# Performance work log

Measured on AMD Instinct MI355X. Metric: run time of the kernel, lower is better.

## Reference

```python
import jax, jax.numpy as jnp
import numpy as np

EMBED_DIM = 256
IDX = 3
SLOT_NORM = True
NEG = -9e15


def setup_inputs() -> dict:
    key = jax.random.key(0)
    ks = jax.random.split(key, 7)
    B, S, D, N = 16, 8192, EMBED_DIM, 64
    return {
        "input_embedding": jax.random.normal(ks[0], (B, S, D), dtype=jnp.float32),
        "mask": jax.random.randint(ks[1], (B, N, S), 0, 2, dtype=jnp.int32),
        "Wv": jax.random.normal(ks[2], (D, D), dtype=jnp.float32) * 0.02,
        "bv": jax.random.normal(ks[3], (D,), dtype=jnp.float32) * 0.02,
        "Wk": jax.random.normal(ks[4], (D, D), dtype=jnp.float32) * 0.02,
        "bk": jax.random.normal(ks[5], (D,), dtype=jnp.float32) * 0.02,
        "queries": jax.random.normal(ks[6], (N, D), dtype=jnp.float32) * 0.02,
    }


def reference(input_embedding, mask, Wv, bv, Wk, bk, queries):
    # values/keys: [B, S, D] (torch Linear: x @ W.T + b)
    values = jnp.einsum("bsd,ed->bse", input_embedding, Wv) + bv
    keys = jnp.einsum("bsd,ed->bse", input_embedding, Wk) + bk
    # attn_logits: [B, N, S]
    logits = jnp.einsum("nd,bsd->bns", queries, keys) / jnp.sqrt(
        jnp.asarray(EMBED_DIM, dtype=keys.dtype)
    )
    logits = jnp.where(mask == 0, jnp.asarray(NEG, dtype=logits.dtype), logits)
    if SLOT_NORM:
        attn = jax.nn.softmax(logits, axis=-2)  # normalize over slots
        attn = attn / jnp.sum(attn, axis=-1, keepdims=True)
    else:
        attn = jax.nn.softmax(logits, axis=-1)
    attention = attn[:, IDX, :][:, None, :]  # [B, 1, S]
    out = jnp.matmul(attention, values)  # [B, 1, D]
    return out, attention
```

## Files before the change

kernel.cpp:

```cpp
#include <hip/hip_runtime.h>


#define B_ 16
#define S_ 8192
#define D_ 256
#define N_ 64
#define NEG_ (-9e15f)
#define LSTR 264

typedef __attribute__((ext_vector_type(8))) short s8_t;
typedef __attribute__((ext_vector_type(4))) float f4_t;
typedef unsigned int u32;
typedef unsigned short u16;

__device__ __forceinline__ u16 f2bf(float f) {
  u32 u = __builtin_bit_cast(u32, f);
  u += 0x7fffu + ((u >> 16) & 1u);
  return (u16)(u >> 16);
}
__device__ __forceinline__ float bflo(u32 p) { return __builtin_bit_cast(float, p << 16); }
__device__ __forceinline__ float bfhi(u32 p) { return __builtin_bit_cast(float, p & 0xffff0000u); }

__global__ void prep_qk(const float* __restrict__ queries, const float* __restrict__ Wk,
                        const float* __restrict__ bk, u16* __restrict__ qp,
                        float* __restrict__ qb) {
  const int n = blockIdx.x, d = threadIdx.x;
  const float* q = &queries[n * D_];
  float acc = 0.f;
  for (int e = 0; e < D_; ++e) acc = fmaf(q[e], Wk[e * D_ + d], acc);
  qp[n * D_ + d] = f2bf(acc);
  if (d == 0) {
    float s = 0.f;
    for (int e = 0; e < D_; ++e) s = fmaf(q[e], bk[e], s);
    qb[n] = s;
  }
}

__global__ __launch_bounds__(256, 2) void attn_main(
    const float* __restrict__ x, const int* __restrict__ mask,
    const u16* __restrict__ qp, const float* __restrict__ qb,
    float* __restrict__ wsum, float* __restrict__ denom, float* __restrict__ att) {
  __shared__ u16 q_lds[N_ * LSTR];
  __shared__ u16 in_lds[64 * LSTR];
  __shared__ u32 pm[4 * 64];

  const int t = threadIdx.x;
  const int lane = t & 63;
  const int w = t >> 6;
  const int c15 = lane & 15;
  const int g = lane >> 4;
  const int b = blockIdx.y;
  const int sbase = blockIdx.x * 256;

  {
    const int n = t >> 2, q = t & 3;
#pragma unroll
    for (int j = 0; j < 8; ++j)
      *(uint4*)&q_lds[n * LSTR + q * 64 + j * 8] = *(const uint4*)&qp[n * D_ + q * 64 + j * 8];
  }
  float qbv[4];
#pragma unroll
  for (int t4 = 0; t4 < 4; ++t4) qbv[t4] = qb[t4 * 16 + c15];

  f4_t wacc = {0.f, 0.f, 0.f, 0.f};
  float dacc = 0.f;

  for (int tt = 0; tt < 4; ++tt) {
    const int s0 = sbase + tt * 64;
    __syncthreads();
    {
      const int col = (t & 63) * 4;
#pragma unroll
      for (int it = 0; it < 16; ++it) {
        const int row = it * 4 + w;
        const float4 v = *(const float4*)&x[(((long)b * S_) + s0 + row) * D_ + col];
        uint2 h;
        h.x = (u32)f2bf(v.x) | ((u32)f2bf(v.y) << 16);
        h.y = (u32)f2bf(v.z) | ((u32)f2bf(v.w) << 16);
        *(uint2*)&in_lds[row * LSTR + col] = h;
      }
      const int s = t & 63, p = t >> 6;
      const int* mrow = mask + ((long)b * N_ + p * 16) * S_ + s0 + s;
      u32 bits = 0;
#pragma unroll
      for (int i = 0; i < 16; ++i) bits |= (u32)(mrow[i * S_] != 0) << i;
      pm[p * 64 + s] = bits;
    }
    __syncthreads();

    f4_t acc[4] = {{0.f,0.f,0.f,0.f},{0.f,0.f,0.f,0.f},{0.f,0.f,0.f,0.f},{0.f,0.f,0.f,0.f}};
    const u16* arow = &in_lds[(16 * w + c15) * LSTR + g * 8];
    const u16* br0 = &q_lds[(0 + c15) * LSTR + g * 8];
    const u16* br1 = &q_lds[(16 + c15) * LSTR + g * 8];
    const u16* br2 = &q_lds[(32 + c15) * LSTR + g * 8];
    const u16* br3 = &q_lds[(48 + c15) * LSTR + g * 8];
#pragma unroll
    for (int c = 0; c < 8; ++c) {
      const s8_t a = *(const s8_t*)&arow[c * 32];
      acc[0] = __builtin_amdgcn_mfma_f32_16x16x32_bf16(a, *(const s8_t*)&br0[c * 32], acc[0], 0, 0, 0);
      acc[1] = __builtin_amdgcn_mfma_f32_16x16x32_bf16(a, *(const s8_t*)&br1[c * 32], acc[1], 0, 0, 0);
      acc[2] = __builtin_amdgcn_mfma_f32_16x16x32_bf16(a, *(const s8_t*)&br2[c * 32], acc[2], 0, 0, 0);
      acc[3] = __builtin_amdgcn_mfma_f32_16x16x32_bf16(a, *(const s8_t*)&br3[c * 32], acc[3], 0, 0, 0);
    }

    float unorm[4];
#pragma unroll
    for (int r = 0; r < 4; ++r) {
      const int sl = 16 * w + g * 4 + r;
      float lf[4];
#pragma unroll
      for (int t4 = 0; t4 < 4; ++t4)
        lf[t4] = ((pm[t4 * 64 + sl] >> c15) & 1) ? (acc[t4][r] + qbv[t4]) * 0.0625f : NEG_;
      float m = fmaxf(fmaxf(lf[0], lf[1]), fmaxf(lf[2], lf[3]));
      m = fmaxf(m, __shfl_xor(m, 1));
      m = fmaxf(m, __shfl_xor(m, 2));
      m = fmaxf(m, __shfl_xor(m, 4));
      m = fmaxf(m, __shfl_xor(m, 8));
      const float e0 = __expf(lf[0] - m);
      float sm = e0 + __expf(lf[1] - m) + __expf(lf[2] - m) + __expf(lf[3] - m);
      sm += __shfl_xor(sm, 1);
      sm += __shfl_xor(sm, 2);
      sm += __shfl_xor(sm, 4);
      sm += __shfl_xor(sm, 8);
      const float e3 = __shfl(e0, (lane & 48) | 3);
      unorm[r] = e3 / sm;
    }
    if (c15 == 3) {
      f4_t u = {unorm[0], unorm[1], unorm[2], unorm[3]};
      *(f4_t*)&att[(long)b * S_ + s0 + 16 * w + g * 4] = u;
    }
#pragma unroll
    for (int r = 0; r < 4; ++r) {
#pragma unroll
      for (int gg = 0; gg < 4; ++gg) {
        const float a_s = __shfl(unorm[r], gg * 16);
        const uint2 h = *(const uint2*)&in_lds[(16 * w + gg * 4 + r) * LSTR + lane * 4];
        wacc[0] = fmaf(a_s, bflo(h.x), wacc[0]);
        wacc[1] = fmaf(a_s, bfhi(h.x), wacc[1]);
        wacc[2] = fmaf(a_s, bflo(h.y), wacc[2]);
        wacc[3] = fmaf(a_s, bfhi(h.y), wacc[3]);
        dacc += a_s;
      }
    }
  }
#pragma unroll
  for (int j = 0; j < 4; ++j) atomicAdd(&wsum[b * D_ + lane * 4 + j], wacc[j]);
  if (lane == 0) atomicAdd(&denom[b], dacc);
}

__global__ void finalize_k(const float* __restrict__ wsum, const float* __restrict__ denom,
                           const float* __restrict__ Wv, const float* __restrict__ bv,
                           float* __restrict__ out, float* __restrict__ att) {
  __shared__ float wl[D_];
  const int b = blockIdx.x, t = threadIdx.x;
  wl[t] = wsum[b * D_ + t];
  __syncthreads();
  const float dn = denom[b];
  float o = 0.f;
  const float* wr = &Wv[t * D_];
  for (int e = 0; e < D_; ++e) o = fmaf(wl[e], wr[e], o);
  out[b * D_ + t] = o / dn + bv[t];
  const float inv = 1.0f / dn;
  for (int s = t; s < S_; s += 256) att[(long)b * S_ + s] *= inv;
}

extern "C" void kernel_launch(void* const* d_in, const int* in_sizes, int n_in,
                              void* d_out, int out_size, void* d_ws, size_t ws_size,
                              hipStream_t stream) {
  const float* x = (const float*)d_in[0];
  const int* mask = (const int*)d_in[1];
  const float* Wv = (const float*)d_in[2];
  const float* bv = (const float*)d_in[3];
  const float* Wk = (const float*)d_in[4];
  const float* bk = (const float*)d_in[5];
  const float* queries = (const float*)d_in[6];

  char* ws = (char*)d_ws;
  u16* qp = (u16*)ws;
  float* qb = (float*)(ws + 32768);
  float* wsum = (float*)(ws + 33024);
  float* denom = (float*)(ws + 49408);
  float* out = (float*)d_out;
  float* att = out + B_ * D_;

  hipMemsetAsync(wsum, 0, 16384 + 64, stream);
  prep_qk<<<N_, D_, 0, stream>>>(queries, Wk, bk, qp, qb);
  attn_main<<<dim3(32, B_), 256, 0, stream>>>(x, mask, qp, qb, wsum, denom, att);
  finalize_k<<<B_, D_, 0, stream>>>(wsum, denom, Wv, bv, out, att);
}
```

Before: 270.3 us.

## Split mask packing into own kernel, drop LDS staging of x, retile attention

Mask bits are now packed into 64-bit words per position by a separate kernel. The main kernel then reads x directly from global memory into MFMA operands and for the weighted sum, removing the bf16 LDS staging of the input. The query matrix is pre-swizzled into MFMA fragment order in prep_qk, and blocks handle 128 positions instead of 256, giving twice as many blocks. Finalize is also split across more blocks for the attention rescale. The main kernel reads x from global twice (L2 likely serves the second read), and the weighted sum now uses fp32 x rather than its bf16-rounded copy.

```diff
diff --git a/kernel.cpp b/kernel.cpp
--- a/kernel.cpp
+++ b/kernel.cpp
@@ -6,7 +6,6 @@
 #define D_ 256
 #define N_ 64
 #define NEG_ (-9e15f)
-#define LSTR 264
 
 typedef __attribute__((ext_vector_type(8))) short s8_t;
 typedef __attribute__((ext_vector_type(4))) float f4_t;
@@ -18,31 +17,50 @@
   u += 0x7fffu + ((u >> 16) & 1u);
   return (u16)(u >> 16);
 }
-__device__ __forceinline__ float bflo(u32 p) { return __builtin_bit_cast(float, p << 16); }
-__device__ __forceinline__ float bfhi(u32 p) { return __builtin_bit_cast(float, p & 0xffff0000u); }
+
+__global__ void pack_mask(const int* __restrict__ mask, uint2* __restrict__ pm) {
+  const int b = blockIdx.y;
+  const int s = blockIdx.x * 256 + threadIdx.x;
+  const int* mp = mask + (long)b * N_ * S_ + s;
+  u32 lo = 0, hi = 0;
+#pragma unroll 16
+  for (int n = 0; n < 32; ++n) lo |= (u32)(mp[n * S_] != 0) << n;
+#pragma unroll 16
+  for (int n = 0; n < 32; ++n) hi |= (u32)(mp[(32 + n) * S_] != 0) << n;
+  uint2 r; r.x = lo; r.y = hi;
+  pm[b * S_ + s] = r;
+}
 
 __global__ void prep_qk(const float* __restrict__ queries, const float* __restrict__ Wk,
-                        const float* __restrict__ bk, u16* __restrict__ qp,
+                        const float* __restrict__ bk, u16* __restrict__ qf,
                         float* __restrict__ qb) {
+  __shared__ float ql[D_];
+  __shared__ float rb[D_];
   const int n = blockIdx.x, d = threadIdx.x;
-  const float* q = &queries[n * D_];
-  float acc = 0.f;
-  for (int e = 0; e < D_; ++e) acc = fmaf(q[e], Wk[e * D_ + d], acc);
-  qp[n * D_ + d] = f2bf(acc);
-  if (d == 0) {
-    float s = 0.f;
-    for (int e = 0; e < D_; ++e) s = fmaf(q[e], bk[e], s);
-    qb[n] = s;
-  }
-}
-
-__global__ __launch_bounds__(256, 2) void attn_main(
-    const float* __restrict__ x, const int* __restrict__ mask,
-    const u16* __restrict__ qp, const float* __restrict__ qb,
+  const float qv = queries[n * D_ + d];
+  ql[d] = qv;
+  rb[d] = qv * bk[d];
+  __syncthreads();
+  float a0 = 0.f, a1 = 0.f, a2 = 0.f, a3 = 0.f;
+#pragma unroll 4
+  for (int e = 0; e < D_; e += 4) {
+    a0 = fmaf(ql[e + 0], Wk[(e + 0) * D_ + d], a0);
+    a1 = fmaf(ql[e + 1], Wk[(e + 1) * D_ + d], a1);
+    a2 = fmaf(ql[e + 2], Wk[(e + 2) * D_ + d], a2);
+    a3 = fmaf(ql[e + 3], Wk[(e + 3) * D_ + d], a3);
+  }
+  const float acc = (a0 + a1) + (a2 + a3);
+  const int t4 = n >> 4, c15 = n & 15, c = d >> 5, g = (d >> 3) & 3, j = d & 7;
+  qf[((t4 * 8 + c) * 64 + g * 16 + c15) * 8 + j] = f2bf(acc);
+  for (int s = 128; s > 0; s >>= 1) { __syncthreads(); if (d < s) rb[d] += rb[d + s]; }
+  if (d == 0) qb[n] = rb[0];
+}
+
+__global__ __launch_bounds__(256) void attn_main(
+    const float* __restrict__ x, const uint2* __restrict__ pm,
+    const u16* __restrict__ qf, const float* __restrict__ qb,
     float* __restrict__ wsum, float* __restrict__ denom, float* __restrict__ att) {
-  __shared__ u16 q_lds[N_ * LSTR];
-  __shared__ u16 in_lds[64 * LSTR];
-  __shared__ u32 pm[4 * 64];
+  __shared__ __align__(16) u16 q_lds[N_ * D_];
 
   const int t = threadIdx.x;
   const int lane = t & 63;
@@ -50,74 +68,57 @@
   const int c15 = lane & 15;
   const int g = lane >> 4;
   const int b = blockIdx.y;
-  const int sbase = blockIdx.x * 256;
-
-  {
-    const int n = t >> 2, q = t & 3;
-#pragma unroll
-    for (int j = 0; j < 8; ++j)
-      *(uint4*)&q_lds[n * LSTR + q * 64 + j * 8] = *(const uint4*)&qp[n * D_ + q * 64 + j * 8];
-  }
-  float qbv[4];
-#pragma unroll
-  for (int t4 = 0; t4 < 4; ++t4) qbv[t4] = qb[t4 * 16 + c15];
-
-  f4_t wacc = {0.f, 0.f, 0.f, 0.f};
+  const int sbase = blockIdx.x * 128;
+
+#pragma unroll
+  for (int i = 0; i < 8; ++i)
+    ((uint4*)q_lds)[t + 256 * i] = ((const uint4*)qf)[t + 256 * i];
+
+  float qbv0 = qb[c15], qbv1 = qb[16 + c15], qbv2 = qb[32 + c15], qbv3 = qb[48 + c15];
+
+  float wacc[4][4] = {{0.f,0.f,0.f,0.f},{0.f,0.f,0.f,0.f},{0.f,0.f,0.f,0.f},{0.f,0.f,0.f,0.f}};
   float dacc = 0.f;
-
-  for (int tt = 0; tt < 4; ++tt) {
+  __syncthreads();
+
+  for (int tt = 0; tt < 2; ++tt) {
     const int s0 = sbase + tt * 64;
-    __syncthreads();
-    {
-      const int col = (t & 63) * 4;
-#pragma unroll
-      for (int it = 0; it < 16; ++it) {
-        const int row = it * 4 + w;
-        const float4 v = *(const float4*)&x[(((long)b * S_) + s0 + row) * D_ + col];
-        uint2 h;
-        h.x = (u32)f2bf(v.x) | ((u32)f2bf(v.y) << 16);
-        h.y = (u32)f2bf(v.z) | ((u32)f2bf(v.w) << 16);
-        *(uint2*)&in_lds[row * LSTR + col] = h;
-      }
-      const int s = t & 63, p = t >> 6;
-      const int* mrow = mask + ((long)b * N_ + p * 16) * S_ + s0 + s;
-      u32 bits = 0;
-#pragma unroll
-      for (int i = 0; i < 16; ++i) bits |= (u32)(mrow[i * S_] != 0) << i;
-      pm[p * 64 + s] = bits;
-    }
-    __syncthreads();
-
-    f4_t acc[4] = {{0.f,0.f,0.f,0.f},{0.f,0.f,0.f,0.f},{0.f,0.f,0.f,0.f},{0.f,0.f,0.f,0.f}};
-    const u16* arow = &in_lds[(16 * w + c15) * LSTR + g * 8];
-    const u16* br0 = &q_lds[(0 + c15) * LSTR + g * 8];
-    const u16* br1 = &q_lds[(16 + c15) * LSTR + g * 8];
-    const u16* br2 = &q_lds[(32 + c15) * LSTR + g * 8];
-    const u16* br3 = &q_lds[(48 + c15) * LSTR + g * 8];
+    uint2 mm[4];
+#pragma unroll
+    for (int r = 0; r < 4; ++r) mm[r] = pm[b * S_ + s0 + 16 * w + g * 4 + r];
+
+    const float* xrow = x + (((long)b * S_) + s0 + 16 * w + c15) * D_ + g * 8;
+    f4_t acc0 = {0.f,0.f,0.f,0.f}, acc1 = {0.f,0.f,0.f,0.f};
+    f4_t acc2 = {0.f,0.f,0.f,0.f}, acc3 = {0.f,0.f,0.f,0.f};
 #pragma unroll
     for (int c = 0; c < 8; ++c) {
-      const s8_t a = *(const s8_t*)&arow[c * 32];
-      acc[0] = __builtin_amdgcn_mfma_f32_16x16x32_bf16(a, *(const s8_t*)&br0[c * 32], acc[0], 0, 0, 0);
-      acc[1] = __builtin_amdgcn_mfma_f32_16x16x32_bf16(a, *(const s8_t*)&br1[c * 32], acc[1], 0, 0, 0);
-      acc[2] = __builtin_amdgcn_mfma_f32_16x16x32_bf16(a, *(const s8_t*)&br2[c * 32], acc[2], 0, 0, 0);
-      acc[3] = __builtin_amdgcn_mfma_f32_16x16x32_bf16(a, *(const s8_t*)&br3[c * 32], acc[3], 0, 0, 0);
+      const float4 v0 = *(const float4*)(xrow + c * 32);
+      const float4 v1 = *(const float4*)(xrow + c * 32 + 4);
+      s8_t a;
+      u32* ap = (u32*)&a;
+      ap[0] = (u32)f2bf(v0.x) | ((u32)f2bf(v0.y) << 16);
+      ap[1] = (u32)f2bf(v0.z) | ((u32)f2bf(v0.w) << 16);
+      ap[2] = (u32)f2bf(v1.x) | ((u32)f2bf(v1.y) << 16);
+      ap[3] = (u32)f2bf(v1.z) | ((u32)f2bf(v1.w) << 16);
+      acc0 = __builtin_amdgcn_mfma_f32_16x16x32_bf16(a, *(const s8_t*)&q_lds[((0 * 8 + c) * 64 + lane) * 8], acc0, 0, 0, 0);
+      acc1 = __builtin_amdgcn_mfma_f32_16x16x32_bf16(a, *(const s8_t*)&q_lds[((1 * 8 + c) * 64 + lane) * 8], acc1, 0, 0, 0);
+      acc2 = __builtin_amdgcn_mfma_f32_16x16x32_bf16(a, *(const s8_t*)&q_lds[((2 * 8 + c) * 64 + lane) * 8], acc2, 0, 0, 0);
+      acc3 = __builtin_amdgcn_mfma_f32_16x16x32_bf16(a, *(const s8_t*)&q_lds[((3 * 8 + c) * 64 + lane) * 8], acc3, 0, 0, 0);
     }
 
     float unorm[4];
 #pragma unroll
     for (int r = 0; r < 4; ++r) {
-      const int sl = 16 * w + g * 4 + r;
-      float lf[4];
-#pragma unroll
-      for (int t4 = 0; t4 < 4; ++t4)
-        lf[t4] = ((pm[t4 * 64 + sl] >> c15) & 1) ? (acc[t4][r] + qbv[t4]) * 0.0625f : NEG_;
-      float m = fmaxf(fmaxf(lf[0], lf[1]), fmaxf(lf[2], lf[3]));
+      const float lf0 = ((mm[r].x >> c15) & 1)        ? (acc0[r] + qbv0) * 0.0625f : NEG_;
+      const float lf1 = ((mm[r].x >> (16 + c15)) & 1) ? (acc1[r] + qbv1) * 0.0625f : NEG_;
+      const float lf2 = ((mm[r].y >> c15) & 1)        ? (acc2[r] + qbv2) * 0.0625f : NEG_;
+      const float lf3 = ((mm[r].y >> (16 + c15)) & 1) ? (acc3[r] + qbv3) * 0.0625f : NEG_;
+      float m = fmaxf(fmaxf(lf0, lf1), fmaxf(lf2, lf3));
       m = fmaxf(m, __shfl_xor(m, 1));
       m = fmaxf(m, __shfl_xor(m, 2));
       m = fmaxf(m, __shfl_xor(m, 4));
       m = fmaxf(m, __shfl_xor(m, 8));
-      const float e0 = __expf(lf[0] - m);
-      float sm = e0 + __expf(lf[1] - m) + __expf(lf[2] - m) + __expf(lf[3] - m);
+      const float e0 = __expf(lf0 - m);
+      float sm = e0 + __expf(lf1 - m) + __expf(lf2 - m) + __expf(lf3 - m);
       sm += __shfl_xor(sm, 1);
       sm += __shfl_xor(sm, 2);
       sm += __shfl_xor(sm, 4);
@@ -129,39 +130,67 @@
       f4_t u = {unorm[0], unorm[1], unorm[2], unorm[3]};
       *(f4_t*)&att[(long)b * S_ + s0 + 16 * w + g * 4] = u;
     }
+
+    const float* wrow = x + (((long)b * S_) + s0 + 16 * w + g * 4) * D_ + c15 * 16;
 #pragma unroll
     for (int r = 0; r < 4; ++r) {
-#pragma unroll
-      for (int gg = 0; gg < 4; ++gg) {
-        const float a_s = __shfl(unorm[r], gg * 16);
-        const uint2 h = *(const uint2*)&in_lds[(16 * w + gg * 4 + r) * LSTR + lane * 4];
-        wacc[0] = fmaf(a_s, bflo(h.x), wacc[0]);
-        wacc[1] = fmaf(a_s, bfhi(h.x), wacc[1]);
-        wacc[2] = fmaf(a_s, bflo(h.y), wacc[2]);
-        wacc[3] = fmaf(a_s, bfhi(h.y), wacc[3]);
-        dacc += a_s;
+      const float a_s = unorm[r];
+#pragma unroll
+      for (int k = 0; k < 4; ++k) {
+        const float4 v = *(const float4*)(wrow + r * D_ + k * 4);
+        wacc[k][0] = fmaf(a_s, v.x, wacc[k][0]);
+        wacc[k][1] = fmaf(a_s, v.y, wacc[k][1]);
+        wacc[k][2] = fmaf(a_s, v.z, wacc[k][2]);
+        wacc[k][3] = fmaf(a_s, v.w, wacc[k][3]);
       }
-    }
-  }
-#pragma unroll
-  for (int j = 0; j < 4; ++j) atomicAdd(&wsum[b * D_ + lane * 4 + j], wacc[j]);
+      dacc += a_s;
+    }
+  }
+
+#pragma unroll
+  for (int k = 0; k < 4; ++k)
+#pragma unroll
+    for (int j = 0; j < 4; ++j) {
+      wacc[k][j] += __shfl_xor(wacc[k][j], 16);
+      wacc[k][j] += __shfl_xor(wacc[k][j], 32);
+    }
+  dacc += __shfl_xor(dacc, 16);
+  dacc += __shfl_xor(dacc, 32);
+
+#pragma unroll
+  for (int j = 0; j < 4; ++j) {
+    const float lo = (g & 1) ? wacc[1][j] : wacc[0][j];
+    const float hi = (g & 1) ? wacc[3][j] : wacc[2][j];
+    const float val = (g & 2) ? hi : lo;
+    atomicAdd(&wsum[b * D_ + c15 * 16 + g * 4 + j], val);
+  }
   if (lane == 0) atomicAdd(&denom[b], dacc);
 }
 
 __global__ void finalize_k(const float* __restrict__ wsum, const float* __restrict__ denom,
                            const float* __restrict__ Wv, const float* __restrict__ bv,
                            float* __restrict__ out, float* __restrict__ att) {
-  __shared__ float wl[D_];
-  const int b = blockIdx.x, t = threadIdx.x;
-  wl[t] = wsum[b * D_ + t];
-  __syncthreads();
+  const int b = blockIdx.x, t = threadIdx.x, part = blockIdx.y;
   const float dn = denom[b];
-  float o = 0.f;
-  const float* wr = &Wv[t * D_];
-  for (int e = 0; e < D_; ++e) o = fmaf(wl[e], wr[e], o);
-  out[b * D_ + t] = o / dn + bv[t];
-  const float inv = 1.0f / dn;
-  for (int s = t; s < S_; s += 256) att[(long)b * S_ + s] *= inv;
+  if (part == 0) {
+    __shared__ float wl[D_];
+    wl[t] = wsum[b * D_ + t];
+    __syncthreads();
+    const float4* wr = (const float4*)&Wv[t * D_];
+    const float4* wv = (const float4*)wl;
+    float s0 = 0.f, s1 = 0.f, s2 = 0.f, s3 = 0.f;
+#pragma unroll 8
+    for (int e = 0; e < 64; ++e) {
+      const float4 a = wv[e], w4 = wr[e];
+      s0 = fmaf(a.x, w4.x, s0); s1 = fmaf(a.y, w4.y, s1);
+      s2 = fmaf(a.z, w4.z, s2); s3 = fmaf(a.w, w4.w, s3);
+    }
+    out[b * D_ + t] = ((s0 + s1) + (s2 + s3)) / dn + bv[t];
+  } else {
+    const float inv = 1.0f / dn;
+    const int s = (part - 1) * 256 + t;
+    att[(long)b * S_ + s] *= inv;
+  }
 }
 
 extern "C" void kernel_launch(void* const* d_in, const int* in_sizes, int n_in,
@@ -176,15 +205,17 @@
   const float* queries = (const float*)d_in[6];
 
   char* ws = (char*)d_ws;
-  u16* qp = (u16*)ws;
-  float* qb = (float*)(ws + 32768);
-  float* wsum = (float*)(ws + 33024);
-  float* denom = (float*)(ws + 49408);
+  float* wsum = (float*)ws;
+  float* denom = (float*)(ws + 16384);
+  float* qb = (float*)(ws + 16448);
+  u16* qf = (u16*)(ws + 17472);
+  uint2* pm = (uint2*)(ws + 50240);
   float* out = (float*)d_out;
   float* att = out + B_ * D_;
 
-  hipMemsetAsync(wsum, 0, 16384 + 64, stream);
-  prep_qk<<<N_, D_, 0, stream>>>(queries, Wk, bk, qp, qb);
-  attn_main<<<dim3(32, B_), 256, 0, stream>>>(x, mask, qp, qb, wsum, denom, att);
-  finalize_k<<<B_, D_, 0, stream>>>(wsum, denom, Wv, bv, out, att);
-}
+  hipMemsetAsync(wsum, 0, 16448, stream);
+  pack_mask<<<dim3(32, B_), 256, 0, stream>>>(mask, pm);
+  prep_qk<<<N_, D_, 0, stream>>>(queries, Wk, bk, qf, qb);
+  attn_main<<<dim3(64, B_), 256, 0, stream>>>(x, pm, qf, qb, wsum, denom, att);
+  finalize_k<<<dim3(B_, 33), 256, 0, stream>>>(wsum, denom, Wv, bv, out, att);
+}
```

New measurement: 348.8 us. 1.29x slower.
